# Kernel tuning notes

Hardware: AMD Instinct MI355X
Metric: run time of the kernel (lower is better)

## Reference

```python
import jax, jax.numpy as jnp
import numpy as np

GAMMAK = 1.0 / 256.0  # 1/(2*d) so kernel values don't underflow for unit-gaussian data


def setup_inputs() -> dict:
    key = jax.random.key(0)
    k1, k2, k3, k4, k5 = jax.random.split(key, 5)
    N, d = 8192, 128
    X = jax.random.normal(k1, (N, d), dtype=jnp.float32)
    y = jax.random.normal(k2, (N - 1, d), dtype=jnp.float32)
    y_next = jax.random.normal(k3, (N - 1, d), dtype=jnp.float32)
    # reset_transform initializes R=eye, t=0; perturb slightly for nontrivial math
    R = jnp.eye(d, dtype=jnp.float32) + 0.01 * jax.random.normal(k4, (d, d), dtype=jnp.float32)
    t = 0.01 * jax.random.normal(k5, (d, 1), dtype=jnp.float32)
    return {"X": X, "y": y, "y_next": y_next, "R": R, "t": t}


def reference(X, y, y_next, R, t):
    # _transform_pts: (R @ y.T + t).T == y @ R.T + t.squeeze()
    yt = y @ R.T + t[:, 0]            # (N-1, d)
    Xb = X[:-1]                        # (N-1, d) kernel base points
    # pairwise_sqeuclidean(Xb, yt), clamped at 0
    sq = jnp.clip(
        jnp.sum(Xb * Xb, axis=1)[:, None]
        + jnp.sum(yt * yt, axis=1)[None, :]
        - 2.0 * (Xb @ yt.T),
        0.0, None,
    )                                  # (N-1, N-1)
    G = jnp.exp(-GAMMAK * sq)
    # diag(1/rowsum) @ G  ==  G / rowsum[:, None]  (avoids explicit NxN diagonal)
    y_pred = (G / jnp.sum(G, axis=1, keepdims=True)) @ X[1:]  # (N-1, d)
    return y_pred
```

## Files before the change

### kernel.cpp

```cpp
#include <hip/hip_runtime.h>
#include <hip/hip_bf16.h>


#define LOG2E 1.44269504088896340736f
#define KNEG (-(1.0f/256.0f)*LOG2E)
#define KA2C (2.0f*(1.0f/256.0f)*LOG2E)

typedef __attribute__((ext_vector_type(4)))  float f32x4;
typedef __attribute__((ext_vector_type(16))) float f32x16;
typedef __attribute__((ext_vector_type(8)))  short bf16x8;

__device__ __forceinline__ unsigned short f2bf(float f) {
  unsigned u = __builtin_bit_cast(unsigned, f);
  u = (u + 0x7fffu + ((u >> 16) & 1u)) >> 16;
  return (unsigned short)u;
}
__device__ __forceinline__ unsigned pk2bf(float a, float b) {
  __hip_bfloat162 h = __float22bfloat162_rn(float2{a, b});
  unsigned u;
  __builtin_memcpy(&u, &h, 4);
  return u;
}
__device__ __forceinline__ bf16x8 pack8(float4 p0, float4 p1) {
  uint4 u;
  u.x = pk2bf(p0.x, p0.y); u.y = pk2bf(p0.z, p0.w);
  u.z = pk2bf(p1.x, p1.y); u.w = pk2bf(p1.z, p1.w);
  return __builtin_bit_cast(bf16x8, u);
}
__device__ __forceinline__ float fast_exp2(float x) {
#if __has_builtin(__builtin_amdgcn_exp2f)
  return __builtin_amdgcn_exp2f(x);
#else
  return exp2f(x);
#endif
}
__device__ __forceinline__ void gl2lds16(const void* g, void* l) {
  __builtin_amdgcn_global_load_lds((const __attribute__((address_space(1))) unsigned int*)g,
                                   (__attribute__((address_space(3))) unsigned int*)l, 16, 0, 0);
}
__device__ __forceinline__ f32x16 mfma_32x32x16(bf16x8 a, bf16x8 b, f32x16 c) {
  return __builtin_amdgcn_mfma_f32_32x32x16_bf16(a, b, c, 0, 0, 0);
}

#define T_STRIDE 34816
#define V_OFF    18432

__global__ __launch_bounds__(64) void k_prep(const float* __restrict__ y,
                                             const float* __restrict__ R,
                                             const float* __restrict__ t,
                                             const float* __restrict__ X,
                                             unsigned short* __restrict__ ctp) {
  __shared__ char slice[8704];
  const int task = blockIdx.x;
  const int ln = threadIdx.x;
  const int l = ln & 31, h = ln >> 5;

  if (task < 256) {
    unsigned short* ytt = (unsigned short*)slice;
    float* ynf = (float*)(slice + 8448);
    const int T = task >> 1, jcw = task & 1;
    const int rw = task * 32;
    bf16x8 af[8];
    {
      int row = rw + l; if (row > 8190) row = 8190;
      const float* yr = y + (size_t)row * 128;
#pragma unroll
      for (int kc = 0; kc < 8; ++kc) {
        float4 p0 = *(const float4*)(yr + kc*16 + 8*h);
        float4 p1 = *(const float4*)(yr + kc*16 + 8*h + 4);
        af[kc] = pack8(p0, p1);
      }
    }
    f32x16 ac[4];
#pragma unroll
    for (int cc=0; cc<4; ++cc)
#pragma unroll
      for (int i=0;i<16;++i) ac[cc][i] = 0.f;
#pragma unroll
    for (int cc=0; cc<4; ++cc) {
      const float* Rr = R + (size_t)(cc*32 + l) * 128;
#pragma unroll
      for (int kc=0; kc<8; ++kc) {
        float4 p0 = *(const float4*)(Rr + kc*16 + 8*h);
        float4 p1 = *(const float4*)(Rr + kc*16 + 8*h + 4);
        ac[cc] = mfma_32x32x16(af[kc], pack8(p0, p1), ac[cc]);
      }
    }
    float tv0 = t[l], tv1 = t[32+l], tv2 = t[64+l], tv3 = t[96+l];
    float v0[16], v1[16], v2[16], v3[16], ssq[16];
#pragma unroll
    for (int r=0;r<16;++r) {
      v0[r]=ac[0][r]+tv0; v1[r]=ac[1][r]+tv1; v2[r]=ac[2][r]+tv2; v3[r]=ac[3][r]+tv3;
      ssq[r] = v0[r]*v0[r] + v1[r]*v1[r] + v2[r]*v2[r] + v3[r]*v3[r];
    }
#pragma unroll
    for (int off=1; off<32; off<<=1)
#pragma unroll
      for (int r=0;r<16;++r) ssq[r] += __shfl_xor(ssq[r], off, 64);
    if (l < 16) {
      int r = l;
      int grow = rw + (r&3) + 8*(r>>2) + 4*h;
      ynf[(r&3) + 8*(r>>2) + 4*h] = (grow >= 8191) ? -1.0e4f : KNEG * ssq[r];
    }
#pragma unroll
    for (int r=0;r<16;++r) {
      int rloc = (r&3) + 8*(r>>2) + 4*h;
      ytt[rloc*132 +   0 + l] = f2bf(KA2C * v0[r]);
      ytt[rloc*132 +  32 + l] = f2bf(KA2C * v1[r]);
      ytt[rloc*132 +  64 + l] = f2bf(KA2C * v2[r]);
      ytt[rloc*132 +  96 + l] = f2bf(KA2C * v3[r]);
    }
    __syncthreads();
    char* base = (char*)ctp + (size_t)T*T_STRIDE;
#pragma unroll
    for (int kc=0;kc<8;++kc) {
      const unsigned short* s = &ytt[l*132 + kc*16 + 8*h];
      uint2 a = *(const uint2*)(s);
      uint2 b = *(const uint2*)(s + 4);
      uint4 o; o.x=a.x; o.y=a.y; o.z=b.x; o.w=b.y;
      *(uint4*)(base + (jcw*9 + kc)*1024 + ln*16) = o;
    }
    {
      float yn = ynf[l];
      unsigned short hi = f2bf(yn);
      float hif = __builtin_bit_cast(float, (unsigned)hi << 16);
      unsigned short lo = f2bf(yn - hif);
      uint4 o; o.x = (h == 0) ? ((unsigned)hi | ((unsigned)lo << 16)) : 0u;
      o.y = 0u; o.z = 0u; o.w = 0u;
      *(uint4*)(base + (jcw*9 + 8)*1024 + ln*16) = o;
    }
  } else {
    unsigned short* xs = (unsigned short*)slice;
    const int tv_ = task - 256;
    const int T2 = tv_ >> 1, half = tv_ & 1;
    const int xr0 = T2*64 + half*32 + 1;
    {
      int rl = ln >> 1, ch2 = ln & 1;
      int row = xr0 + rl; if (row > 8191) row = 8191;
      const float* src = X + (size_t)row*128 + ch2*64;
      unsigned short* dst = xs + rl*136 + ch2*64;
#pragma unroll
      for (int i=0;i<8;++i) {
        float4 p0 = *(const float4*)(src + i*8);
        float4 p1 = *(const float4*)(src + i*8 + 4);
        uint4 w;
        w.x = pk2bf(p0.x, p0.y); w.y = pk2bf(p0.z, p0.w);
        w.z = pk2bf(p1.x, p1.y); w.w = pk2bf(p1.z, p1.w);
        *(uint4*)(dst + i*8) = w;
      }
    }
    __syncthreads();
    char* base = (char*)ctp + (size_t)T2*T_STRIDE + V_OFF;
#pragma unroll
    for (int ch=0; ch<8; ++ch) {
      int jcl = ch >> 2, cc = ch & 3;
      int lr0 = jcl*16 + 8*h;
      int c = cc*32 + l;
      uint4 o;
      o.x = (unsigned)xs[(lr0+0)*136 + c] | ((unsigned)xs[(lr0+1)*136 + c] << 16);
      o.y = (unsigned)xs[(lr0+2)*136 + c] | ((unsigned)xs[(lr0+3)*136 + c] << 16);
      o.z = (unsigned)xs[(lr0+4)*136 + c] | ((unsigned)xs[(lr0+5)*136 + c] << 16);
      o.w = (unsigned)xs[(lr0+6)*136 + c] | ((unsigned)xs[(lr0+7)*136 + c] << 16);
      int jc16 = half*2 + jcl;
      *(uint4*)(base + (jc16*4 + cc)*1024 + ln*16) = o;
    }
  }
}

__global__ __launch_bounds__(256, 3) void k_main(
    const float* __restrict__ X,
    const unsigned short* __restrict__ ctp,
    float* __restrict__ accp,
    float* __restrict__ rsp,
    int js) {
  __shared__ unsigned short stg[T_STRIDE/2];
  __shared__ unsigned short gls[4*32*68];
  const int tid = threadIdx.x;
  const int wv = tid >> 6, ln = tid & 63;
  const int l = ln & 31, h = ln >> 5;
  const int row = blockIdx.x*128 + wv*32 + l;

  bf16x8 qf[9];
  {
    const float* xr = X + (size_t)row * 128;
#pragma unroll
    for (int kc=0;kc<8;++kc) {
      float4 p0 = *(const float4*)(xr + kc*16 + 8*h);
      float4 p1 = *(const float4*)(xr + kc*16 + 8*h + 4);
      qf[kc] = pack8(p0, p1);
    }
    uint4 o; o.x = (h == 0) ? 0x3F803F80u : 0u; o.y = 0u; o.z = 0u; o.w = 0u;
    qf[8] = __builtin_bit_cast(bf16x8, o);
  }
  f32x16 acc[4];
#pragma unroll
  for (int cc=0;cc<4;++cc)
#pragma unroll
    for (int i=0;i<16;++i) acc[cc][i]=0.f;
  float rs = 0.f;
  const int sp = blockIdx.y;
  const int Tbeg = (sp * 128) / js;
  const int Tend = ((sp + 1) * 128) / js;
  for (int T = Tbeg; T < Tend; ++T) {
    __syncthreads();
    {
      const char* cb = (const char*)ctp + (size_t)T*T_STRIDE;
#pragma unroll
      for (int i=0;i<9;++i) {
        int c = wv + 4*i;
        if (c < 34) gl2lds16(cb + c*1024 + ln*16, (char*)stg + c*1024);
      }
    }
    __syncthreads();
#pragma unroll
    for (int jc=0; jc<2; ++jc) {
      f32x16 sa;
#pragma unroll
      for (int i=0;i<16;++i) sa[i]=0.f;
#pragma unroll
      for (int kc=0;kc<9;++kc) {
        bf16x8 a = *(const bf16x8*)((const char*)stg + (jc*9+kc)*1024 + ln*16);
        sa = mfma_32x32x16(a, qf[kc], sa);
      }
#pragma unroll
      for (int rg=0; rg<4; ++rg) {
        float g0 = fast_exp2(sa[rg*4+0]);
        float g1 = fast_exp2(sa[rg*4+1]);
        float g2 = fast_exp2(sa[rg*4+2]);
        float g3 = fast_exp2(sa[rg*4+3]);
        rs += (g0+g1) + (g2+g3);
        uint2 w; w.x = pk2bf(g0, g1); w.y = pk2bf(g2, g3);
        int j0 = jc*32 + 8*rg + 4*h;
        *(uint2*)&gls[(wv*32+l)*68 + j0] = w;
      }
      __builtin_amdgcn_wave_barrier();
#pragma unroll
      for (int jj=0; jj<2; ++jj) {
        int jc16 = jc*2 + jj;
        const unsigned short* gp = &gls[(wv*32+l)*68 + jc16*16 + 8*h];
        uint2 g0 = *(const uint2*)(gp);
        uint2 g1 = *(const uint2*)(gp + 4);
        uint4 gv; gv.x=g0.x; gv.y=g0.y; gv.z=g1.x; gv.w=g1.y;
        bf16x8 pb = __builtin_bit_cast(bf16x8, gv);
#pragma unroll
        for (int cc=0;cc<4;++cc) {
          bf16x8 a2 = *(const bf16x8*)((const char*)stg + V_OFF + (jc16*4+cc)*1024 + ln*16);
          acc[cc] = mfma_32x32x16(a2, pb, acc[cc]);
        }
      }
      __builtin_amdgcn_wave_barrier();
    }
  }
  rs += __shfl_xor(rs, 32, 64);
  if (h == 0) rsp[(size_t)sp*8192 + row] = rs;
#pragma unroll
  for (int cc=0;cc<4;++cc)
#pragma unroll
    for (int r=0;r<16;++r) {
      int c = cc*32 + (r&3) + 8*(r>>2) + 4*h;
      accp[((size_t)sp*128 + c)*8192 + row] = acc[cc][r];
    }
}

__global__ __launch_bounds__(256) void k_fin(const float* __restrict__ accp,
                                             const float* __restrict__ rsp,
                                             float* __restrict__ out,
                                             int js) {
  __shared__ float tr[64*36];
  __shared__ float rinv[64];
  const int tid = threadIdx.x;
  const int r0 = blockIdx.x * 64;
  const int c0 = blockIdx.y * 32;
  if (tid < 64) {
    float s = 0.f;
    for (int sp=0; sp<js; ++sp) s += rsp[(size_t)sp*8192 + r0 + tid];
    rinv[tid] = 1.f / s;
  }
  const int rq = tid & 15, cg = tid >> 4;
  float v[2][4];
#pragma unroll
  for (int cc=0;cc<2;++cc)
#pragma unroll
    for (int k=0;k<4;++k) v[cc][k]=0.f;
#pragma unroll 4
  for (int sp=0; sp<js; ++sp) {
    const float* base = accp + ((size_t)sp*128 + c0 + cg*2)*8192 + r0 + rq*4;
    float4 p0 = *(const float4*)(base);
    float4 p1 = *(const float4*)(base + 8192);
    v[0][0]+=p0.x; v[0][1]+=p0.y; v[0][2]+=p0.z; v[0][3]+=p0.w;
    v[1][0]+=p1.x; v[1][1]+=p1.y; v[1][2]+=p1.z; v[1][3]+=p1.w;
  }
  __syncthreads();
#pragma unroll
  for (int cc=0;cc<2;++cc)
#pragma unroll
    for (int k=0;k<4;++k)
      tr[(rq*4+k)*36 + cg*2+cc] = v[cc][k] * rinv[rq*4+k];
  __syncthreads();
  {
    int r = tid >> 2, q = tid & 3;
    int grow = r0 + r;
    if (grow < 8191) {
      float* dst = out + (size_t)grow*128 + c0 + q*8;
      const float* s2 = &tr[r*36 + q*8];
      *(float4*)(dst)     = *(const float4*)(s2);
      *(float4*)(dst + 4) = *(const float4*)(s2 + 4);
    }
  }
}

extern "C" void kernel_launch(void* const* d_in, const int* in_sizes, int n_in,
                              void* d_out, int out_size, void* d_ws, size_t ws_size,
                              hipStream_t stream) {
  const float* X = (const float*)d_in[0];
  const float* y = (const float*)d_in[1];
  const float* R = (const float*)d_in[3];
  const float* t = (const float*)d_in[4];
  float* out = (float*)d_out;
  char* ws = (char*)d_ws;

  unsigned short* ctp = (unsigned short*)ws;
  size_t rspoff = (size_t)128 * T_STRIDE;
  float* rsp  = (float*)(ws + rspoff);
  size_t accoff = rspoff + 512*1024;
  float* accp = (float*)(ws + accoff);

  int js = 12;
  while (js > 1 && accoff + (size_t)js*128*8192*4 > ws_size) js >>= 1;

  k_prep<<<dim3(512), dim3(64), 0, stream>>>(y, R, t, X, ctp);
  k_main<<<dim3(64, js), dim3(256), 0, stream>>>(X, ctp, accp, rsp, js);
  k_fin<<<dim3(128, 4), dim3(256), 0, stream>>>(accp, rsp, out, js);
}
```

Before: 134.6 us.

## Prefetch next tile during compute and replace LDS P-transpose with permlane32 swap

```diff
diff --git a/kernel.cpp b/kernel.cpp
--- a/kernel.cpp
+++ b/kernel.cpp
@@ -40,6 +40,20 @@
 }
 __device__ __forceinline__ f32x16 mfma_32x32x16(bf16x8 a, bf16x8 b, f32x16 c) {
   return __builtin_amdgcn_mfma_f32_32x32x16_bf16(a, b, c, 0, 0, 0);
+}
+__device__ __forceinline__ void pl32swap(unsigned &a, unsigned &b) {
+#if __has_builtin(__builtin_amdgcn_permlane32_swap)
+  auto r = __builtin_amdgcn_permlane32_swap((int)a, (int)b, false, false);
+  a = (unsigned)r[0];
+  b = (unsigned)r[1];
+#else
+  unsigned pa = (unsigned)__shfl_xor((int)a, 32, 64);
+  unsigned pb = (unsigned)__shfl_xor((int)b, 32, 64);
+  bool hi = (threadIdx.x & 32) != 0;
+  unsigned na = hi ? pb : a;
+  unsigned nb = hi ? b  : pa;
+  a = na; b = nb;
+#endif
 }
 
 #define T_STRIDE 34816
@@ -174,7 +188,6 @@
     float* __restrict__ rsp,
     int js) {
   __shared__ unsigned short stg[T_STRIDE/2];
-  __shared__ unsigned short gls[4*32*68];
   const int tid = threadIdx.x;
   const int wv = tid >> 6, ln = tid & 63;
   const int l = ln & 31, h = ln >> 5;
@@ -201,54 +214,85 @@
   const int sp = blockIdx.y;
   const int Tbeg = (sp * 128) / js;
   const int Tend = ((sp + 1) * 128) / js;
+
+  auto dosm = [&](const f32x16& sa, unsigned wx[4], unsigned wy[4]) {
+#pragma unroll
+    for (int rg=0; rg<4; ++rg) {
+      float g0 = fast_exp2(sa[rg*4+0]);
+      float g1 = fast_exp2(sa[rg*4+1]);
+      float g2 = fast_exp2(sa[rg*4+2]);
+      float g3 = fast_exp2(sa[rg*4+3]);
+      rs += (g0+g1) + (g2+g3);
+      wx[rg] = pk2bf(g0, g1);
+      wy[rg] = pk2bf(g2, g3);
+    }
+  };
+  auto dopv = [&](int jcb, unsigned wx[4], unsigned wy[4]) {
+#pragma unroll
+    for (int jj=0; jj<2; ++jj) {
+      unsigned ax = wx[2*jj], bx = wx[2*jj+1];
+      unsigned ay = wy[2*jj], by = wy[2*jj+1];
+      pl32swap(ax, bx);
+      pl32swap(ay, by);
+      uint4 gv; gv.x = ax; gv.y = ay; gv.z = bx; gv.w = by;
+      bf16x8 pb = __builtin_bit_cast(bf16x8, gv);
+#pragma unroll
+      for (int cc=0;cc<4;++cc) {
+        bf16x8 a2 = *(const bf16x8*)((const char*)stg + V_OFF + ((jcb+jj)*4+cc)*1024 + ln*16);
+        acc[cc] = mfma_32x32x16(a2, pb, acc[cc]);
+      }
+    }
+  };
+
+  {
+    const char* cb = (const char*)ctp + (size_t)Tbeg*T_STRIDE;
+#pragma unroll
+    for (int i=0;i<9;++i) {
+      int c = wv + 4*i;
+      if (c < 34) gl2lds16(cb + c*1024 + ln*16, (char*)stg + c*1024);
+    }
+  }
+  __syncthreads();
+
   for (int T = Tbeg; T < Tend; ++T) {
+    const bool pf = (T+1 < Tend);
+    const char* nb = (const char*)ctp + (size_t)(T+1)*T_STRIDE;
+
+    f32x16 sa0, sa1;
+#pragma unroll
+    for (int i=0;i<16;++i) { sa0[i]=0.f; sa1[i]=0.f; }
+#pragma unroll
+    for (int kc=0;kc<9;++kc) {
+      bf16x8 a0 = *(const bf16x8*)((const char*)stg + kc*1024 + ln*16);
+      sa0 = mfma_32x32x16(a0, qf[kc], sa0);
+    }
+#pragma unroll
+    for (int kc=0;kc<9;++kc) {
+      bf16x8 a1 = *(const bf16x8*)((const char*)stg + (9+kc)*1024 + ln*16);
+      sa1 = mfma_32x32x16(a1, qf[kc], sa1);
+    }
+    unsigned wx0[4], wy0[4], wx1[4], wy1[4];
+    dosm(sa0, wx0, wy0);
+
     __syncthreads();
-    {
-      const char* cb = (const char*)ctp + (size_t)T*T_STRIDE;
-#pragma unroll
-      for (int i=0;i<9;++i) {
+    if (pf) {
+#pragma unroll
+      for (int i=0;i<5;++i) {
         int c = wv + 4*i;
-        if (c < 34) gl2lds16(cb + c*1024 + ln*16, (char*)stg + c*1024);
-      }
-    }
+        if (c < 18) gl2lds16(nb + c*1024 + ln*16, (char*)stg + c*1024);
+      }
+    }
+    dosm(sa1, wx1, wy1);
+    dopv(0, wx0, wy0);
+    dopv(2, wx1, wy1);
+
     __syncthreads();
-#pragma unroll
-    for (int jc=0; jc<2; ++jc) {
-      f32x16 sa;
-#pragma unroll
-      for (int i=0;i<16;++i) sa[i]=0.f;
-#pragma unroll
-      for (int kc=0;kc<9;++kc) {
-        bf16x8 a = *(const bf16x8*)((const char*)stg + (jc*9+kc)*1024 + ln*16);
-        sa = mfma_32x32x16(a, qf[kc], sa);
-      }
-#pragma unroll
-      for (int rg=0; rg<4; ++rg) {
-        float g0 = fast_exp2(sa[rg*4+0]);
-        float g1 = fast_exp2(sa[rg*4+1]);
-        float g2 = fast_exp2(sa[rg*4+2]);
-        float g3 = fast_exp2(sa[rg*4+3]);
-        rs += (g0+g1) + (g2+g3);
-        uint2 w; w.x = pk2bf(g0, g1); w.y = pk2bf(g2, g3);
-        int j0 = jc*32 + 8*rg + 4*h;
-        *(uint2*)&gls[(wv*32+l)*68 + j0] = w;
-      }
-      __builtin_amdgcn_wave_barrier();
-#pragma unroll
-      for (int jj=0; jj<2; ++jj) {
-        int jc16 = jc*2 + jj;
-        const unsigned short* gp = &gls[(wv*32+l)*68 + jc16*16 + 8*h];
-        uint2 g0 = *(const uint2*)(gp);
-        uint2 g1 = *(const uint2*)(gp + 4);
-        uint4 gv; gv.x=g0.x; gv.y=g0.y; gv.z=g1.x; gv.w=g1.y;
-        bf16x8 pb = __builtin_bit_cast(bf16x8, gv);
-#pragma unroll
-        for (int cc=0;cc<4;++cc) {
-          bf16x8 a2 = *(const bf16x8*)((const char*)stg + V_OFF + (jc16*4+cc)*1024 + ln*16);
-          acc[cc] = mfma_32x32x16(a2, pb, acc[cc]);
-        }
-      }
-      __builtin_amdgcn_wave_barrier();
+    if (pf) {
+#pragma unroll
+      for (int i=0;i<4;++i) {
+        int c = 18 + wv + 4*i;
+        gl2lds16(nb + c*1024 + ln*16, (char*)stg + c*1024);
+      }
     }
   }
   rs += __shfl_xor(rs, 32, 64);
```

Measured after the change: 130.2 us (median of 2 runs). 3.2% less time.
